# Kernel optimization log

Hardware: AMD Instinct MI355X
Metric: run time of the kernel (lower is better)

## Reference

```python
import jax, jax.numpy as jnp
import numpy as np

N = 20000; E = 320000; IN = 128; OUT = 128; H = 8; D = 16
SQRT_DK = float(D) ** 0.5

def setup_inputs() -> dict:
    key = jax.random.key(0)
    ks = jax.random.split(key, 20)
    s = 0.05
    glorot = (6.0 / (D + D)) ** 0.5
    inp = dict(
        h_a=jax.random.normal(ks[0], (N, IN), jnp.float32),
        h_b=jax.random.normal(ks[1], (N, IN), jnp.float32),
        Wk=jax.random.normal(ks[2], (2, IN, OUT), jnp.float32) * s,
        bk=jnp.zeros((2, OUT), jnp.float32),
        Wq=jax.random.normal(ks[3], (2, IN, OUT), jnp.float32) * s,
        bq=jnp.zeros((2, OUT), jnp.float32),
        Wv=jax.random.normal(ks[4], (2, IN, OUT), jnp.float32) * s,
        bv=jnp.zeros((2, OUT), jnp.float32),
        Wa=jax.random.normal(ks[5], (2, OUT, OUT), jnp.float32) * s,
        ba=jnp.zeros((2, OUT), jnp.float32),
        rel_att=jax.random.normal(ks[6], (4, H, D, D), jnp.float32) * glorot,
        rel_msg=jax.random.normal(ks[7], (4, H, D, D), jnp.float32) * glorot,
        rel_pri=jnp.ones((4, H), jnp.float32),
        skip=jnp.ones((2,), jnp.float32),
    )
    names = ["src_aa", "dst_aa", "src_ab", "dst_ab", "src_ba", "dst_ba", "src_bb", "dst_bb"]
    for i, name in enumerate(names):
        inp[name] = jax.random.randint(ks[8 + i], (E,), 0, N, jnp.int32)
    return inp

def _relation(h_src, h_dst, src, dst, Wk_t, bk_t, Wq_t, bq_t, Wv_t, bv_t, att, msg, pri):
    # relation-specific K/V transform + Q projection
    k = (h_src @ Wk_t + bk_t).reshape(-1, H, D)
    v = (h_src @ Wv_t + bv_t).reshape(-1, H, D)
    q = (h_dst @ Wq_t + bq_t).reshape(-1, H, D)
    k = jnp.einsum('nhd,hde->nhe', k, att)
    v = jnp.einsum('nhd,hde->nhe', v, msg)
    # edge dot-product score (v_dot_u: q[dst] . k[src]), [E, H]
    score = jnp.einsum('ehd,ehd->eh', q[dst], k[src]) * pri / SQRT_DK
    # edge softmax normalized by dst
    smax = jax.ops.segment_max(score, dst, num_segments=N)
    ex = jnp.exp(score - smax[dst])
    ssum = jax.ops.segment_sum(ex, dst, num_segments=N)
    attn = ex / ssum[dst]
    # weighted scatter-aggregate, [N, H, D]
    return jax.ops.segment_sum(v[src] * attn[:, :, None], dst, num_segments=N)

def reference(h_a, h_b, Wk, bk, Wq, bq, Wv, bv, Wa, ba, rel_att, rel_msg, rel_pri, skip,
              src_aa, dst_aa, src_ab, dst_ab, src_ba, dst_ba, src_bb, dst_bb):
    agg_aa = _relation(h_a, h_a, src_aa, dst_aa, Wk[0], bk[0], Wq[0], bq[0], Wv[0], bv[0], rel_att[0], rel_msg[0], rel_pri[0])
    agg_ab = _relation(h_a, h_b, src_ab, dst_ab, Wk[0], bk[0], Wq[1], bq[1], Wv[0], bv[0], rel_att[1], rel_msg[1], rel_pri[1])
    agg_ba = _relation(h_b, h_a, src_ba, dst_ba, Wk[1], bk[1], Wq[0], bq[0], Wv[1], bv[1], rel_att[2], rel_msg[2], rel_pri[2])
    agg_bb = _relation(h_b, h_b, src_bb, dst_bb, Wk[1], bk[1], Wq[1], bq[1], Wv[1], bv[1], rel_att[3], rel_msg[3], rel_pri[3])
    # cross_reducer='mean' over the 2 relations targeting each node type
    t_a = (0.5 * (agg_aa + agg_ba)).reshape(N, OUT)
    t_b = (0.5 * (agg_ab + agg_bb)).reshape(N, OUT)
    al_a = jax.nn.sigmoid(skip[0])
    al_b = jax.nn.sigmoid(skip[1])
    new_a = al_a * (t_a @ Wa[0] + ba[0]) + (1.0 - al_a) * h_a
    new_b = al_b * (t_b @ Wa[1] + ba[1]) + (1.0 - al_b) * h_b
    return new_a, new_b
```

## Files before the change

kernel.cpp:

```cpp
#include <hip/hip_runtime.h>
#include <stdint.h>

#define N_NODES 20000
#define N_EDGES 320000
#define C 128
#define H 8
#define D 16
#define SLOT 64
#define NRANGE 5000
#define RANGES2 10000
#define CAP2 80

#define P_CVT 2500
#define P_ZERO 625
#define P_PACK 128
#define P_FUSE 32
#define MB_TOTAL 8130

typedef short s16x8 __attribute__((ext_vector_type(8)));
typedef float f32x4 __attribute__((ext_vector_type(4)));

__device__ __forceinline__ unsigned short f2bf(float f) {
    unsigned int b = __float_as_uint(f);
    b += 0x7fffu + ((b >> 16) & 1u);
    return (unsigned short)(b >> 16);
}
__device__ __forceinline__ float bf2f(unsigned int u) {
    return __uint_as_float(u << 16);
}
__device__ __forceinline__ float bf_lo(unsigned int u) {
    return __uint_as_float(u << 16);
}
__device__ __forceinline__ float bf_hi(unsigned int u) {
    return __uint_as_float(u & 0xffff0000u);
}

__global__ __launch_bounds__(256) void prep_k(const float* __restrict__ h_a, const float* __restrict__ h_b,
                                              unsigned short* __restrict__ oa, unsigned short* __restrict__ ob,
                                              const float* __restrict__ Wq, const float* __restrict__ Wa,
                                              unsigned short* __restrict__ Wqt, unsigned short* __restrict__ Wat,
                                              const float* __restrict__ Wk, const float* __restrict__ Wv,
                                              const float* __restrict__ bk, const float* __restrict__ bv,
                                              const float* __restrict__ att, const float* __restrict__ msg,
                                              unsigned short* __restrict__ Wkt, unsigned short* __restrict__ Wvt,
                                              float* __restrict__ bkt, float* __restrict__ bvt,
                                              int* __restrict__ cur) {
    __shared__ float sa[D * D], sm[D * D];
    int bid = blockIdx.x;
    int tid = threadIdx.x;
    if (bid < P_CVT) {
        int i = (bid * 256 + tid) * 4;
        float4 va = *(const float4*)(h_a + i);
        float4 vb = *(const float4*)(h_b + i);
        ushort4 ua = { f2bf(va.x), f2bf(va.y), f2bf(va.z), f2bf(va.w) };
        ushort4 ub = { f2bf(vb.x), f2bf(vb.y), f2bf(vb.z), f2bf(vb.w) };
        *(ushort4*)(oa + i) = ua;
        *(ushort4*)(ob + i) = ub;
        return;
    }
    bid -= P_CVT;
    if (bid < P_ZERO) {
        int i = bid * 256 + tid;
        if (i < 160000) ((int4*)cur)[i] = make_int4(0, 0, 0, 0);
        return;
    }
    bid -= P_ZERO;
    if (bid < P_PACK) {
        int n = bid;
        int t = tid >> 7, i = tid & 127;
        Wqt[(t * C + n) * C + i] = f2bf(Wq[(t * C + i) * C + n]);
        Wat[(t * C + n) * C + i] = f2bf(Wa[(t * C + i) * C + n]);
        return;
    }
    bid -= P_PACK;
    {
        int r = bid >> 3, h = bid & 7;
        int t = r >> 1;
        if (tid < D * D) {
            sa[tid] = att[(r * H + h) * D * D + tid];
            sm[tid] = msg[(r * H + h) * D * D + tid];
        }
        __syncthreads();
        int i = tid & 127;
        for (int e = (tid >> 7); e < D; e += 2) {
            float sk = 0.f, sv = 0.f;
            for (int d = 0; d < D; ++d) {
                sk += Wk[(t * C + i) * C + h * D + d] * sa[d * D + e];
                sv += Wv[(t * C + i) * C + h * D + d] * sm[d * D + e];
            }
            Wkt[(r * C + h * D + e) * C + i] = f2bf(sk);
            Wvt[(r * C + h * D + e) * C + i] = f2bf(sv);
        }
        if (tid < D) {
            int e = tid;
            float sk = 0.f, sv = 0.f;
            for (int d = 0; d < D; ++d) {
                sk += bk[t * C + h * D + d] * sa[d * D + e];
                sv += bv[t * C + h * D + d] * sm[d * D + e];
            }
            bkt[r * C + h * D + e] = sk;
            bvt[r * C + h * D + e] = sv;
        }
    }
}

__global__ __launch_bounds__(256) void mega_k(const int* __restrict__ s0, const int* __restrict__ s1,
                                              const int* __restrict__ s2, const int* __restrict__ s3,
                                              const int* __restrict__ d0, const int* __restrict__ d1,
                                              const int* __restrict__ d2, const int* __restrict__ d3,
                                              int* __restrict__ cur, unsigned short* __restrict__ part,
                                              const unsigned short* __restrict__ ha,
                                              const unsigned short* __restrict__ hb,
                                              const unsigned short* __restrict__ Wqt,
                                              const unsigned short* __restrict__ Wkt,
                                              const unsigned short* __restrict__ Wvt,
                                              const float* __restrict__ bq,
                                              const float* __restrict__ bkt,
                                              const float* __restrict__ bvt,
                                              unsigned short* __restrict__ Qa,
                                              unsigned short* __restrict__ Qb,
                                              unsigned short* __restrict__ Kall,
                                              unsigned short* __restrict__ Vall) {
    int bid = blockIdx.x;
    int part_id = -1, proj_id = -1;
    if (bid < 8125) {
        int p = bid / 13, o = bid - p * 13;
        if (o < 8) part_id = p * 8 + o;
        else       proj_id = p * 5 + (o - 8);
    } else {
        proj_id = 3125 + (bid - 8125);
    }

    if (part_id >= 0) {
        int r = part_id / 1250;
        int eb = part_id - r * 1250;
        int e = eb * 256 + threadIdx.x;
        const int* dd = (r == 0) ? d0 : (r == 1) ? d1 : (r == 2) ? d2 : d3;
        const int* ss = (r == 0) ? s0 : (r == 1) ? s1 : (r == 2) ? s2 : s3;
        int d = dd[e];
        int range = d >> 1;
        int pos = atomicAdd(&cur[(r * RANGES2 + range) * 16], 1);
        if (pos < CAP2)
            part[((size_t)(r * RANGES2 + range)) * CAP2 + pos] =
                (unsigned short)(ss[e] | ((d & 1) << 15));
        return;
    }
    int j = proj_id / 313;
    int xb = proj_id - j * 313;
    const unsigned short* A;
    const unsigned short* Wt;
    const float* bias;
    unsigned short* Out;
    if (j < 2) {
        A = j ? hb : ha; Wt = Wqt + j * C * C; bias = bq + j * C; Out = j ? Qb : Qa;
    } else if (j < 6) {
        int r = j - 2;
        A = (r < 2) ? ha : hb; Wt = Wkt + r * C * C; bias = bkt + r * C;
        Out = Kall + (size_t)r * N_NODES * C;
    } else {
        int r = j - 6;
        A = (r < 2) ? ha : hb; Wt = Wvt + r * C * C; bias = bvt + r * C;
        Out = Vall + (size_t)r * N_NODES * C;
    }
    int wid = threadIdx.x >> 6, l = threadIdx.x & 63;
    int row_base = xb * 64 + wid * 16;
    int lm = l & 15, q = l >> 4;
    f32x4 acc[8] = {};
    int arow = row_base + lm;
    if (arow >= N_NODES) arow = N_NODES - 1;
    const s16x8* Ap = (const s16x8*)(A + (size_t)arow * C);
#pragma unroll
    for (int kc = 0; kc < 4; ++kc) {
        s16x8 af = Ap[kc * 4 + q];
#pragma unroll
        for (int t = 0; t < 8; ++t) {
            s16x8 bf = *(const s16x8*)(Wt + (t * 16 + lm) * C + kc * 32 + q * 8);
            acc[t] = __builtin_amdgcn_mfma_f32_16x16x32_bf16(af, bf, acc[t], 0, 0, 0);
        }
    }
#pragma unroll
    for (int t = 0; t < 8; ++t) {
        int col = t * 16 + lm;
        float b = bias[col];
#pragma unroll
        for (int i = 0; i < 4; ++i) {
            int row = row_base + q * 4 + i;
            if (row < N_NODES) Out[(size_t)row * C + col] = f2bf(acc[t][i] + b);
        }
    }
}

__global__ __launch_bounds__(256) void final_mm(const unsigned short* __restrict__ AggAll,
                                                const unsigned short* __restrict__ WatAll,
                                                const float* __restrict__ baAll,
                                                const float* __restrict__ skip,
                                                const float* __restrict__ h_a,
                                                const float* __restrict__ h_b,
                                                float* __restrict__ OutAll) {
    int ty = blockIdx.y;
    const unsigned short* Agg = AggAll + (size_t)ty * N_NODES * C;
    const unsigned short* Wat = WatAll + ty * C * C;
    const float* ba = baAll + ty * C;
    const float* h_orig = ty ? h_b : h_a;
    float* Out = OutAll + (size_t)ty * N_NODES * C;
    int wid = threadIdx.x >> 6, l = threadIdx.x & 63;
    int row_base = blockIdx.x * 64 + wid * 16;
    int lm = l & 15, q = l >> 4;
    f32x4 acc[8] = {};
    int arow = row_base + lm;
    if (arow >= N_NODES) arow = N_NODES - 1;
    const s16x8* Ap = (const s16x8*)(Agg + (size_t)arow * C);
#pragma unroll
    for (int kc = 0; kc < 4; ++kc) {
        s16x8 af = Ap[kc * 4 + q];
#pragma unroll
        for (int t = 0; t < 8; ++t) {
            s16x8 bf = *(const s16x8*)(Wat + (t * 16 + lm) * C + kc * 32 + q * 8);
            acc[t] = __builtin_amdgcn_mfma_f32_16x16x32_bf16(af, bf, acc[t], 0, 0, 0);
        }
    }
    float al = 1.f / (1.f + __expf(-skip[ty]));
#pragma unroll
    for (int t = 0; t < 8; ++t) {
        int col = t * 16 + lm;
        float b = ba[col];
#pragma unroll
        for (int i = 0; i < 4; ++i) {
            int row = row_base + q * 4 + i;
            if (row < N_NODES)
                Out[(size_t)row * C + col] = al * (acc[t][i] + b) + (1.f - al) * h_orig[(size_t)row * C + col];
        }
    }
}

__global__ __launch_bounds__(256) void node_p2(const int* __restrict__ cur,
                                               const unsigned short* __restrict__ part,
                                               const unsigned int* __restrict__ Kall,
                                               const unsigned int* __restrict__ Vall,
                                               const float* __restrict__ pri,
                                               const unsigned int* __restrict__ Qa,
                                               const unsigned int* __restrict__ Qb,
                                               unsigned int* __restrict__ agg) {
    __shared__ unsigned short slot[2][4][SLOT];
    __shared__ int cnt[2][4];
    int g = blockIdx.x;
    int type = (g >= NRANGE) ? 1 : 0;
    int range = g - type * NRANGE;
    int relA = type ? 1 : 0;
    int relB = type ? 3 : 2;
    if (threadIdx.x < 8) ((int*)cnt)[threadIdx.x] = 0;
    __syncthreads();
#pragma unroll
    for (int rr = 0; rr < 2; ++rr) {
        int rel = rr ? relB : relA;
#pragma unroll
        for (int seg = 0; seg < 2; ++seg) {
            int r2 = range * 2 + seg;
            int c = cur[(rel * RANGES2 + r2) * 16];
            if (c > CAP2) c = CAP2;
            const unsigned short* pp = part + ((size_t)(rel * RANGES2 + r2)) * CAP2;
            for (int i = threadIdx.x; i < c; i += 256) {
                unsigned int rec = pp[i];
                int dof = 2 * seg + (rec >> 15);
                int p = atomicAdd(&cnt[rr][dof], 1);
                if (p < SLOT) slot[rr][dof][p] = (unsigned short)(rec & 0x7fffu);
            }
        }
    }
    __syncthreads();

    int wid = threadIdx.x >> 6, l = threadIdx.x & 63;
    int eg = l >> 4;
    int j  = l & 15;
    int hg = j >> 1;
    int dof = wid;
    int n = range * 4 + dof;
    const unsigned int* Q32 = type ? Qb : Qa;
    uint4 qv = *(const uint4*)(Q32 + (size_t)n * 64 + j * 4);
    float q0 = bf_lo(qv.x), q1 = bf_hi(qv.x), q2 = bf_lo(qv.y), q3 = bf_hi(qv.y);
    float q4 = bf_lo(qv.z), q5 = bf_hi(qv.z), q6 = bf_lo(qv.w), q7 = bf_hi(qv.w);
    float out[8] = {};

#pragma unroll 1
    for (int rr = 0; rr < 2; ++rr) {
        int rel = rr ? relB : relA;
        const char* Kb = (const char*)(Kall + (size_t)rel * N_NODES * 64);
        const char* Vb = (const char*)(Vall + (size_t)rel * N_NODES * 64);
        float pv = pri[rel * 8 + hg] * 0.25f;
        int deg = cnt[rr][dof];
        if (deg > SLOT) deg = SLOT;
        float m = -1e30f, sum = 0.f;
        float acc[8] = {};
        for (int base = 0; base < deg; base += 16) {
            float s[4];
            uint4 vv[4];
#pragma unroll
            for (int i = 0; i < 4; ++i) {
                int idx = base + i * 4 + eg;
                float d = -1e30f;
                uint4 v = {0u, 0u, 0u, 0u};
                if (idx < deg) {
                    unsigned off = ((unsigned)slot[rr][dof][idx] << 8) | ((unsigned)j << 4);
                    uint4 kv = *(const uint4*)(Kb + off);
                    v = *(const uint4*)(Vb + off);
                    d = q0 * bf_lo(kv.x) + q1 * bf_hi(kv.x)
                      + q2 * bf_lo(kv.y) + q3 * bf_hi(kv.y)
                      + q4 * bf_lo(kv.z) + q5 * bf_hi(kv.z)
                      + q6 * bf_lo(kv.w) + q7 * bf_hi(kv.w);
                    d += __shfl_xor(d, 1);
                    d *= pv;
                }
                s[i] = d;
                vv[i] = v;
            }
            float mloc = fmaxf(fmaxf(s[0], s[1]), fmaxf(s[2], s[3]));
            float mnew = fmaxf(m, mloc);
            float alpha = __expf(m - mnew);
            sum *= alpha;
#pragma unroll
            for (int c2 = 0; c2 < 8; ++c2) acc[c2] *= alpha;
            m = mnew;
#pragma unroll
            for (int i = 0; i < 4; ++i) {
                float ww = (s[i] > -1e29f) ? __expf(s[i] - m) : 0.f;
                sum += ww;
                acc[0] += ww * bf_lo(vv[i].x); acc[1] += ww * bf_hi(vv[i].x);
                acc[2] += ww * bf_lo(vv[i].y); acc[3] += ww * bf_hi(vv[i].y);
                acc[4] += ww * bf_lo(vv[i].z); acc[5] += ww * bf_hi(vv[i].z);
                acc[6] += ww * bf_lo(vv[i].w); acc[7] += ww * bf_hi(vv[i].w);
            }
        }
        float m1 = fmaxf(m, __shfl_xor(m, 16));
        float m2 = fmaxf(m1, __shfl_xor(m1, 32));
        float beta = __expf(m - m2);
        sum *= beta;
        sum += __shfl_xor(sum, 16);
        sum += __shfl_xor(sum, 32);
#pragma unroll
        for (int c2 = 0; c2 < 8; ++c2) {
            float a = acc[c2] * beta;
            a += __shfl_xor(a, 16);
            a += __shfl_xor(a, 32);
            acc[c2] = a;
        }
        if (deg > 0) {
            float rs = 1.f / sum;
#pragma unroll
            for (int c2 = 0; c2 < 8; ++c2) out[c2] += acc[c2] * rs;
        }
    }
    if (eg == 0) {
        uint4 pk;
        pk.x = (unsigned int)f2bf(0.5f * out[0]) | ((unsigned int)f2bf(0.5f * out[1]) << 16);
        pk.y = (unsigned int)f2bf(0.5f * out[2]) | ((unsigned int)f2bf(0.5f * out[3]) << 16);
        pk.z = (unsigned int)f2bf(0.5f * out[4]) | ((unsigned int)f2bf(0.5f * out[5]) << 16);
        pk.w = (unsigned int)f2bf(0.5f * out[6]) | ((unsigned int)f2bf(0.5f * out[7]) << 16);
        *(uint4*)(agg + ((size_t)type * N_NODES + n) * 64 + j * 4) = pk;
    }
}

extern "C" void kernel_launch(void* const* d_in, const int* in_sizes, int n_in,
                              void* d_out, int out_size, void* d_ws, size_t ws_size,
                              hipStream_t stream) {
    const float* h_a  = (const float*)d_in[0];
    const float* h_b  = (const float*)d_in[1];
    const float* Wk   = (const float*)d_in[2];
    const float* bk   = (const float*)d_in[3];
    const float* Wq   = (const float*)d_in[4];
    const float* bq   = (const float*)d_in[5];
    const float* Wv   = (const float*)d_in[6];
    const float* bv   = (const float*)d_in[7];
    const float* Wa   = (const float*)d_in[8];
    const float* ba   = (const float*)d_in[9];
    const float* att  = (const float*)d_in[10];
    const float* msg  = (const float*)d_in[11];
    const float* pri  = (const float*)d_in[12];
    const float* skip = (const float*)d_in[13];
    const int* srcs[4] = {(const int*)d_in[14], (const int*)d_in[16], (const int*)d_in[18], (const int*)d_in[20]};
    const int* dsts[4] = {(const int*)d_in[15], (const int*)d_in[17], (const int*)d_in[19], (const int*)d_in[21]};
    float* out = (float*)d_out;

    char* w = (char*)d_ws;
    auto alloc = [&](size_t bytes) {
        char* p = w;
        w += (bytes + 255) & ~(size_t)255;
        return p;
    };
    unsigned short* ha_bf = (unsigned short*)alloc((size_t)N_NODES * C * 2);
    unsigned short* hb_bf = (unsigned short*)alloc((size_t)N_NODES * C * 2);
    unsigned short* Qa    = (unsigned short*)alloc((size_t)N_NODES * C * 2);
    unsigned short* Qb    = (unsigned short*)alloc((size_t)N_NODES * C * 2);
    unsigned short* Kall  = (unsigned short*)alloc((size_t)4 * N_NODES * C * 2);
    unsigned short* Vall  = (unsigned short*)alloc((size_t)4 * N_NODES * C * 2);
    unsigned short* Wqt   = (unsigned short*)alloc(2 * C * C * 2);
    unsigned short* Wat   = (unsigned short*)alloc(2 * C * C * 2);
    unsigned short* Wkt   = (unsigned short*)alloc(4 * C * C * 2);
    unsigned short* Wvt   = (unsigned short*)alloc(4 * C * C * 2);
    float* bkt            = (float*)alloc(4 * C * 4);
    float* bvt            = (float*)alloc(4 * C * 4);
    int* cur              = (int*)alloc(4 * RANGES2 * 16 * 4);
    unsigned short* part  = (unsigned short*)alloc((size_t)4 * RANGES2 * CAP2 * 2);
    unsigned short* agg   = (unsigned short*)alloc((size_t)2 * N_NODES * C * 2);

    prep_k<<<P_CVT + P_ZERO + P_PACK + P_FUSE, 256, 0, stream>>>(
        h_a, h_b, ha_bf, hb_bf, Wq, Wa, Wqt, Wat,
        Wk, Wv, bk, bv, att, msg, Wkt, Wvt, bkt, bvt, cur);

    mega_k<<<MB_TOTAL, 256, 0, stream>>>(
        srcs[0], srcs[1], srcs[2], srcs[3],
        dsts[0], dsts[1], dsts[2], dsts[3],
        cur, part,
        ha_bf, hb_bf, Wqt, Wkt, Wvt, bq, bkt, bvt,
        Qa, Qb, Kall, Vall);

    node_p2<<<2 * NRANGE, 256, 0, stream>>>(cur, part,
                                            (const unsigned int*)Kall, (const unsigned int*)Vall,
                                            pri,
                                            (const unsigned int*)Qa, (const unsigned int*)Qb,
                                            (unsigned int*)agg);

    final_mm<<<dim3(313, 2), 256, 0, stream>>>(agg, Wat, ba, skip, h_a, h_b, out);
}
```

Measured before the change: 319.7 us.

## Bucket edges by 16-node groups with block-local shared-memory histogram

Replaces the per-edge global atomic partitioning into 2-node ranges with a two-pass block-local counting sort. Each of 80 blocks histograms 16K edges into 1250 buckets of 16 destinations in shared memory, reserves space with one global atomic per bucket, then scatters 32-bit records. This cuts global atomic traffic and shrinks the zeroing work, but node_p2 now reads a 384-entry bucket per 4-node group and filters out three quarters of the records. The partition work also runs on only 80 blocks, which can serialize it against the projection blocks.

```diff
diff --git a/kernel.cpp b/kernel.cpp
--- a/kernel.cpp
+++ b/kernel.cpp
@@ -8,14 +8,17 @@
 #define D 16
 #define SLOT 64
 #define NRANGE 5000
-#define RANGES2 10000
-#define CAP2 80
+#define BUCKETS 1250
+#define BCAP 384
 
 #define P_CVT 2500
-#define P_ZERO 625
+#define P_ZERO 79
 #define P_PACK 128
 #define P_FUSE 32
-#define MB_TOTAL 8130
+#define PB_EDGES 16384
+#define PART_BLOCKS 80
+#define PROJ_BLOCKS 3130
+#define MB_TOTAL (PART_BLOCKS + PROJ_BLOCKS)
 
 typedef short s16x8 __attribute__((ext_vector_type(8)));
 typedef float f32x4 __attribute__((ext_vector_type(4)));
@@ -61,7 +64,7 @@
     bid -= P_CVT;
     if (bid < P_ZERO) {
         int i = bid * 256 + tid;
-        if (i < 160000) ((int4*)cur)[i] = make_int4(0, 0, 0, 0);
+        if (i < 20000) ((int4*)cur)[i] = make_int4(0, 0, 0, 0);
         return;
     }
     bid -= P_ZERO;
@@ -108,7 +111,7 @@
                                               const int* __restrict__ s2, const int* __restrict__ s3,
                                               const int* __restrict__ d0, const int* __restrict__ d1,
                                               const int* __restrict__ d2, const int* __restrict__ d3,
-                                              int* __restrict__ cur, unsigned short* __restrict__ part,
+                                              int* __restrict__ cur, unsigned int* __restrict__ part,
                                               const unsigned short* __restrict__ ha,
                                               const unsigned short* __restrict__ hb,
                                               const unsigned short* __restrict__ Wqt,
@@ -121,30 +124,53 @@
                                               unsigned short* __restrict__ Qb,
                                               unsigned short* __restrict__ Kall,
                                               unsigned short* __restrict__ Vall) {
+    __shared__ int hcnt[BUCKETS];
+    __shared__ int hbase[BUCKETS];
     int bid = blockIdx.x;
-    int part_id = -1, proj_id = -1;
-    if (bid < 8125) {
-        int p = bid / 13, o = bid - p * 13;
-        if (o < 8) part_id = p * 8 + o;
-        else       proj_id = p * 5 + (o - 8);
-    } else {
-        proj_id = 3125 + (bid - 8125);
-    }
-
-    if (part_id >= 0) {
-        int r = part_id / 1250;
-        int eb = part_id - r * 1250;
-        int e = eb * 256 + threadIdx.x;
+    int tid = threadIdx.x;
+
+    if (bid < PART_BLOCKS) {
+        int r  = bid & 3;
+        int pb = bid >> 2;
+        int start = pb * PB_EDGES;
+        int nval = N_EDGES - start;
+        if (nval > PB_EDGES) nval = PB_EDGES;
+        int nq = nval >> 2;
         const int* dd = (r == 0) ? d0 : (r == 1) ? d1 : (r == 2) ? d2 : d3;
         const int* ss = (r == 0) ? s0 : (r == 1) ? s1 : (r == 2) ? s2 : s3;
-        int d = dd[e];
-        int range = d >> 1;
-        int pos = atomicAdd(&cur[(r * RANGES2 + range) * 16], 1);
-        if (pos < CAP2)
-            part[((size_t)(r * RANGES2 + range)) * CAP2 + pos] =
-                (unsigned short)(ss[e] | ((d & 1) << 15));
+        for (int b = tid; b < BUCKETS; b += 256) hcnt[b] = 0;
+        __syncthreads();
+        for (int i = tid; i < nq; i += 256) {
+            int4 d4 = *(const int4*)(dd + start + i * 4);
+            atomicAdd(&hcnt[d4.x >> 4], 1);
+            atomicAdd(&hcnt[d4.y >> 4], 1);
+            atomicAdd(&hcnt[d4.z >> 4], 1);
+            atomicAdd(&hcnt[d4.w >> 4], 1);
+        }
+        __syncthreads();
+        for (int b = tid; b < BUCKETS; b += 256) {
+            int c = hcnt[b];
+            hbase[b] = c ? atomicAdd(&cur[(r * BUCKETS + b) * 16], c) : 0;
+            hcnt[b] = 0;
+        }
+        __syncthreads();
+        for (int i = tid; i < nq; i += 256) {
+            int4 d4 = *(const int4*)(dd + start + i * 4);
+            int4 s4 = *(const int4*)(ss + start + i * 4);
+            int b0 = d4.x >> 4, b1 = d4.y >> 4, b2 = d4.z >> 4, b3 = d4.w >> 4;
+            int i0 = atomicAdd(&hcnt[b0], 1);
+            int i1 = atomicAdd(&hcnt[b1], 1);
+            int i2 = atomicAdd(&hcnt[b2], 1);
+            int i3 = atomicAdd(&hcnt[b3], 1);
+            int p0 = hbase[b0] + i0, p1 = hbase[b1] + i1, p2 = hbase[b2] + i2, p3 = hbase[b3] + i3;
+            if (p0 < BCAP) part[(size_t)(r * BUCKETS + b0) * BCAP + p0] = (unsigned int)s4.x | ((unsigned int)(d4.x & 15) << 15);
+            if (p1 < BCAP) part[(size_t)(r * BUCKETS + b1) * BCAP + p1] = (unsigned int)s4.y | ((unsigned int)(d4.y & 15) << 15);
+            if (p2 < BCAP) part[(size_t)(r * BUCKETS + b2) * BCAP + p2] = (unsigned int)s4.z | ((unsigned int)(d4.z & 15) << 15);
+            if (p3 < BCAP) part[(size_t)(r * BUCKETS + b3) * BCAP + p3] = (unsigned int)s4.w | ((unsigned int)(d4.w & 15) << 15);
+        }
         return;
     }
+    int proj_id = bid - PART_BLOCKS;
     int j = proj_id / 313;
     int xb = proj_id - j * 313;
     const unsigned short* A;
@@ -234,7 +260,7 @@
 }
 
 __global__ __launch_bounds__(256) void node_p2(const int* __restrict__ cur,
-                                               const unsigned short* __restrict__ part,
+                                               const unsigned int* __restrict__ part,
                                                const unsigned int* __restrict__ Kall,
                                                const unsigned int* __restrict__ Vall,
                                                const float* __restrict__ pri,
@@ -250,18 +276,19 @@
     int relB = type ? 3 : 2;
     if (threadIdx.x < 8) ((int*)cnt)[threadIdx.x] = 0;
     __syncthreads();
+    int bkt = range >> 2;
+    int w   = range & 3;
 #pragma unroll
     for (int rr = 0; rr < 2; ++rr) {
         int rel = rr ? relB : relA;
-#pragma unroll
-        for (int seg = 0; seg < 2; ++seg) {
-            int r2 = range * 2 + seg;
-            int c = cur[(rel * RANGES2 + r2) * 16];
-            if (c > CAP2) c = CAP2;
-            const unsigned short* pp = part + ((size_t)(rel * RANGES2 + r2)) * CAP2;
-            for (int i = threadIdx.x; i < c; i += 256) {
-                unsigned int rec = pp[i];
-                int dof = 2 * seg + (rec >> 15);
+        int c = cur[(rel * BUCKETS + bkt) * 16];
+        if (c > BCAP) c = BCAP;
+        const unsigned int* pp = part + (size_t)(rel * BUCKETS + bkt) * BCAP;
+        for (int i = threadIdx.x; i < c; i += 256) {
+            unsigned int rec = pp[i];
+            int dlow = (rec >> 15) & 15;
+            if ((dlow >> 2) == w) {
+                int dof = dlow & 3;
                 int p = atomicAdd(&cnt[rr][dof], 1);
                 if (p < SLOT) slot[rr][dof][p] = (unsigned short)(rec & 0x7fffu);
             }
@@ -398,8 +425,8 @@
     unsigned short* Wvt   = (unsigned short*)alloc(4 * C * C * 2);
     float* bkt            = (float*)alloc(4 * C * 4);
     float* bvt            = (float*)alloc(4 * C * 4);
-    int* cur              = (int*)alloc(4 * RANGES2 * 16 * 4);
-    unsigned short* part  = (unsigned short*)alloc((size_t)4 * RANGES2 * CAP2 * 2);
+    int* cur              = (int*)alloc((size_t)4 * BUCKETS * 16 * 4);
+    unsigned int* part    = (unsigned int*)alloc((size_t)4 * BUCKETS * BCAP * 4);
     unsigned short* agg   = (unsigned short*)alloc((size_t)2 * N_NODES * C * 2);
 
     prep_k<<<P_CVT + P_ZERO + P_PACK + P_FUSE, 256, 0, stream>>>(
```

Measured after the change: 307.8 us. -3.7%, faster.
